# Performance work log

Measured on AMD Instinct MI355X. Metric: run time of the kernel, lower is better.

Reference implementation:

```python
import jax, jax.numpy as jnp
import numpy as np

B, S, HID = 2, 2048, 2048
H, HKV, D = 16, 4, 128

def _rope(x, cos, sin):
    # x: [B,h,S,D]; cos/sin: [1,1,S,D//2]
    d = x.shape[-1] // 2
    x1, x2 = x[..., :d], x[..., d:]
    y1 = x1 * cos + x2 * sin
    y2 = -x1 * sin + x2 * cos
    return jnp.concatenate([y1, y2], axis=-1)

def _rmsnorm(x):
    eps = jnp.finfo(x.dtype).eps
    return x * jax.lax.rsqrt(jnp.mean(jnp.square(x), axis=-1, keepdims=True) + eps)

def setup_inputs() -> dict:
    key = jax.random.key(0)
    ks = jax.random.split(key, 5)
    x = jax.random.normal(ks[0], (B, S, HID), dtype=jnp.float32)
    # realistic rotary tables
    half = D // 2
    inv_freq = 1.0 / (10000.0 ** (jnp.arange(half, dtype=jnp.float32) / half))
    t = jnp.arange(S, dtype=jnp.float32)
    freqs = t[:, None] * inv_freq[None, :]            # [S, D//2]
    cos = jnp.cos(freqs)[None, None]                  # [1,1,S,D//2]
    sin = jnp.sin(freqs)[None, None]
    s = 0.02
    Wq = jax.random.normal(ks[1], (H * D, HID), dtype=jnp.float32) * s
    Wk = jax.random.normal(ks[2], (HKV * D, HID), dtype=jnp.float32) * s
    Wv = jax.random.normal(ks[3], (HKV * D, HID), dtype=jnp.float32) * s
    Wo = jax.random.normal(ks[4], (HID, H * D), dtype=jnp.float32) * s
    return {"x": x, "cos": cos, "sin": sin, "Wq": Wq, "Wk": Wk, "Wv": Wv, "Wo": Wo}

def reference(x, cos, sin, Wq, Wk, Wv, Wo):
    b, s, _ = x.shape
    rep = H // HKV
    q = (x @ Wq.T).reshape(b, s, H, D).transpose(0, 2, 1, 3)      # [B,H,S,D]
    k = (x @ Wk.T).reshape(b, s, HKV, D).transpose(0, 2, 1, 3)    # [B,Hkv,S,D]
    v = (x @ Wv.T).reshape(b, s, HKV, D).transpose(0, 2, 1, 3)
    k = jnp.repeat(k, rep, axis=1)                                # GQA expand
    v = jnp.repeat(v, rep, axis=1)
    q = _rmsnorm(_rope(q, cos, sin))
    k = _rmsnorm(_rope(k, cos, sin))
    scores = jnp.einsum('bhqd,bhkd->bhqk', q, k) * (D ** -0.5)
    causal = jnp.tril(jnp.ones((s, s), dtype=bool))
    scores = jnp.where(causal, scores, -jnp.inf)
    attn = jax.nn.softmax(scores, axis=-1)
    out = jnp.einsum('bhqk,bhkd->bhqd', attn, v)                  # [B,H,S,D]
    out = out.transpose(0, 2, 1, 3).reshape(b, s, H * D)
    return out @ Wo.T
```

## Files before the change

kernel.cpp:

```cpp
#include <hip/hip_runtime.h>
#include <hip/hip_bf16.h>

#define B_  2
#define S_  2048
#define HID_ 2048
#define H_  16
#define HKV_ 4
#define D_  128

typedef __bf16 bf16_t;
typedef bf16_t bf16x8 __attribute__((ext_vector_type(8)));
typedef float f32x4 __attribute__((ext_vector_type(4)));

typedef __attribute__((address_space(3))) unsigned int lds_u32_t;
typedef const __attribute__((address_space(1))) unsigned int glob_u32_t;

__device__ __forceinline__ void gl2lds16(const bf16_t* g, bf16_t* l) {
    __builtin_amdgcn_global_load_lds((glob_u32_t*)g, (lds_u32_t*)l, 16, 0, 0);
}

__device__ __forceinline__ unsigned packbf2(float a, float b) {
    union { bf16_t h[2]; unsigned u; } p;
    p.h[0] = (bf16_t)a;
    p.h[1] = (bf16_t)b;
    return p.u;
}

__global__ void detect_dtype(const unsigned* __restrict__ x, int* __restrict__ flag) {
    int lane = threadIdx.x;
    int c = 0;
#pragma unroll
    for (int i = 0; i < 16; ++i) {
        unsigned w = x[lane * 16 + i];
        unsigned e = (w >> 7) & 0xFF;
        c += (e >= 117 && e <= 137) ? 1 : 0;
    }
#pragma unroll
    for (int m = 1; m < 64; m <<= 1) c += __shfl_xor(c, m, 64);
    if (lane == 0) *flag = (c >= 512) ? 1 : 0;
}

struct Cseg { const void* src; bf16_t* dst; int n8; };

__global__ __launch_bounds__(256) void convert_bf16(Cseg s0, Cseg s1, Cseg s2, Cseg s3,
                                                    const int* __restrict__ flagp) {
    Cseg s = (blockIdx.y == 0) ? s0 : (blockIdx.y == 1) ? s1 : (blockIdx.y == 2) ? s2 : s3;
    const int i = blockIdx.x * 256 + threadIdx.x;
    if (i >= s.n8) return;
    if (*flagp) {
        ((uint4*)s.dst)[i] = ((const uint4*)s.src)[i];
    } else {
        const float4* p = (const float4*)s.src + (size_t)i * 2;
        float4 u = p[0], v = p[1];
        bf16x8 r;
        r[0] = (bf16_t)u.x; r[1] = (bf16_t)u.y; r[2] = (bf16_t)u.z; r[3] = (bf16_t)u.w;
        r[4] = (bf16_t)v.x; r[5] = (bf16_t)v.y; r[6] = (bf16_t)v.z; r[7] = (bf16_t)v.w;
        *(bf16x8*)(s.dst + (size_t)i * 8) = r;
    }
}

__global__ __launch_bounds__(256) void gemm_lds(const bf16_t* __restrict__ A,
                                                const bf16_t* __restrict__ W,
                                                void* __restrict__ C,
                                                int M, int N, int K,
                                                const int* __restrict__ flagp, int osel) {
    __shared__ bf16_t As[128 * 32];
    __shared__ bf16_t Bs[128 * 32];

    const int tid = threadIdx.x;
    const int w = tid >> 6;
    const int lane = tid & 63;
    const int r = lane & 15;
    const int quad = lane >> 4;
    const int m0 = blockIdx.y * 128;
    const int n0 = blockIdx.x * 128;
    const bool of32 = osel && (*flagp == 0);

    const int mh = (w & 1) * 64;
    const int nh = (w >> 1) * 64;

    const int c0 = w * 2;
    const int srow = lane >> 2;
    const int scol = (lane & 3) * 8;
    const bf16_t* Ag0 = A + (size_t)(m0 + c0 * 16 + srow) * K + scol;
    const bf16_t* Ag1 = A + (size_t)(m0 + c0 * 16 + 16 + srow) * K + scol;
    const bf16_t* Wg0 = W + (size_t)(n0 + c0 * 16 + srow) * K + scol;
    const bf16_t* Wg1 = W + (size_t)(n0 + c0 * 16 + 16 + srow) * K + scol;
    bf16_t* Al0 = As + c0 * 512;
    bf16_t* Al1 = As + (c0 + 1) * 512;
    bf16_t* Bl0 = Bs + c0 * 512;
    bf16_t* Bl1 = Bs + (c0 + 1) * 512;

    f32x4 acc[4][4] = {};

    for (int k0 = 0; k0 < K; k0 += 32) {
        __syncthreads();
        gl2lds16(Ag0 + k0, Al0);
        gl2lds16(Ag1 + k0, Al1);
        gl2lds16(Wg0 + k0, Bl0);
        gl2lds16(Wg1 + k0, Bl1);
        __syncthreads();

        bf16x8 a[4], b[4];
#pragma unroll
        for (int mi = 0; mi < 4; ++mi)
            a[mi] = *(const bf16x8*)&As[(mh + mi * 16 + r) * 32 + quad * 8];
#pragma unroll
        for (int ni = 0; ni < 4; ++ni)
            b[ni] = *(const bf16x8*)&Bs[(nh + ni * 16 + r) * 32 + quad * 8];
#pragma unroll
        for (int mi = 0; mi < 4; ++mi)
#pragma unroll
            for (int ni = 0; ni < 4; ++ni)
                acc[mi][ni] = __builtin_amdgcn_mfma_f32_16x16x32_bf16(a[mi], b[ni], acc[mi][ni], 0, 0, 0);
    }

#pragma unroll
    for (int mi = 0; mi < 4; ++mi) {
#pragma unroll
        for (int ni = 0; ni < 4; ++ni) {
#pragma unroll
            for (int g = 0; g < 4; ++g) {
                const int row = m0 + mh + mi * 16 + quad * 4 + g;
                const int col = n0 + nh + ni * 16 + r;
                if (of32) ((float*)C)[(size_t)row * N + col] = acc[mi][ni][g];
                else ((__hip_bfloat16*)C)[(size_t)row * N + col] = __float2bfloat16(acc[mi][ni][g]);
            }
        }
    }
}

template <bool F32>
__device__ __forceinline__ bf16x8 load8(const void* base, size_t off) {
    bf16x8 r;
    if constexpr (F32) {
        const float4* p = (const float4*)((const float*)base + off);
        float4 u = p[0], v = p[1];
        r[0] = (bf16_t)u.x; r[1] = (bf16_t)u.y; r[2] = (bf16_t)u.z; r[3] = (bf16_t)u.w;
        r[4] = (bf16_t)v.x; r[5] = (bf16_t)v.y; r[6] = (bf16_t)v.z; r[7] = (bf16_t)v.w;
    } else {
        r = *(const bf16x8*)((const bf16_t*)base + off);
    }
    return r;
}

template <bool AF32, bool WF32, bool OF32>
__device__ __forceinline__ void gemm_body(const void* __restrict__ A, const void* __restrict__ W,
                                          void* __restrict__ C, int M, int N, int K) {
    const int wave = threadIdx.x >> 6;
    const int lane = threadIdx.x & 63;
    const int r = lane & 15;
    const int quad = lane >> 4;
    const int m0 = blockIdx.y * 64 + wave * 16;
    const int n0 = blockIdx.x * 64;

    f32x4 acc[4] = {};
    const size_t aoff = (size_t)(m0 + r) * K + quad * 8;
    const size_t woff = (size_t)(n0 + r) * K + quad * 8;

    for (int k0 = 0; k0 < K; k0 += 32) {
        bf16x8 a = load8<AF32>(A, aoff + k0);
#pragma unroll
        for (int ns = 0; ns < 4; ++ns) {
            bf16x8 b = load8<WF32>(W, woff + (size_t)(ns * 16) * K + k0);
            acc[ns] = __builtin_amdgcn_mfma_f32_16x16x32_bf16(a, b, acc[ns], 0, 0, 0);
        }
    }

#pragma unroll
    for (int ns = 0; ns < 4; ++ns) {
#pragma unroll
        for (int reg = 0; reg < 4; ++reg) {
            int m = m0 + quad * 4 + reg;
            int n = n0 + ns * 16 + r;
            if constexpr (OF32) ((float*)C)[(size_t)m * N + n] = acc[ns][reg];
            else ((__hip_bfloat16*)C)[(size_t)m * N + n] = __float2bfloat16(acc[ns][reg]);
        }
    }
}

__global__ __launch_bounds__(256) void gemm_bt(const void* __restrict__ A, const void* __restrict__ W,
                                               void* __restrict__ C, int M, int N, int K,
                                               const int* __restrict__ flagp, int mode) {
    const int bf = *flagp;
    if (bf) {
        gemm_body<false, false, false>(A, W, C, M, N, K);
    } else if (mode == 0) {
        gemm_body<true, true, false>(A, W, C, M, N, K);
    } else {
        gemm_body<false, true, true>(A, W, C, M, N, K);
    }
}

__global__ __launch_bounds__(256) void rope_rms(__hip_bfloat16* __restrict__ qk,
                                                const void* __restrict__ cosp,
                                                const void* __restrict__ sinp,
                                                int NH, int ld, const int* __restrict__ flagp) {
    const int bf = *flagp;
    const int wave = threadIdx.x >> 6;
    const int lane = threadIdx.x & 63;
    const int row = blockIdx.x * 4 + wave;
    const int h = row % NH;
    const int bs = row / NH;
    const int s = bs % S_;

    __hip_bfloat16* p = qk + (size_t)bs * ld + h * D_;
    float x1 = __bfloat162float(p[lane]);
    float x2 = __bfloat162float(p[lane + 64]);
    float c, sn, eps;
    if (bf) {
        c   = __bfloat162float(((const __hip_bfloat16*)cosp)[s * 64 + lane]);
        sn  = __bfloat162float(((const __hip_bfloat16*)sinp)[s * 64 + lane]);
        eps = 0.0078125f;
    } else {
        c   = ((const float*)cosp)[s * 64 + lane];
        sn  = ((const float*)sinp)[s * 64 + lane];
        eps = 1.1920929e-07f;
    }
    float y1 = x1 * c + x2 * sn;
    float y2 = x2 * c - x1 * sn;
    float ss = y1 * y1 + y2 * y2;
#pragma unroll
    for (int m = 1; m < 64; m <<= 1) ss += __shfl_xor(ss, m, 64);
    float rinv = rsqrtf(ss * (1.0f / 128.0f) + eps);
    p[lane]      = __float2bfloat16(y1 * rinv);
    p[lane + 64] = __float2bfloat16(y2 * rinv);
}

__global__ __launch_bounds__(256) void k_pack(const __hip_bfloat16* __restrict__ Kin,
                                              bf16_t* __restrict__ Kp) {
    const int idx = blockIdx.x * 256 + threadIdx.x;
    const int sl = idx & 15;
    const int row = (idx >> 4) & 31;
    const int kt = (idx >> 9) & 63;
    const int gy = idx >> 15;
    const int slot = sl ^ (row & 15);
    const int kvh = gy & 3;
    const int bb = gy >> 2;
    const bf16_t* src = (const bf16_t*)Kin + (size_t)(bb * S_ + kt * 32 + row) * 3072 + kvh * D_ + slot * 8;
    *(uint4*)(Kp + (size_t)idx * 8) = *(const uint4*)src;
}

__global__ __launch_bounds__(256) void v_pack(const __hip_bfloat16* __restrict__ V,
                                              unsigned* __restrict__ Vp, int ldv) {
    const int idx = blockIdx.x * 256 + threadIdx.x;
    const int j  = idx & 3;
    const int sl = (idx >> 2) & 3;
    const int d  = (idx >> 4) & 127;
    const int kt = (idx >> 11) & 63;
    const int gy = idx >> 17;
    const int s  = sl ^ ((d >> 1) & 3);
    const int kp = s * 4 + j;
    const int kvh = gy & 3;
    const int b = gy >> 2;
    const unsigned short* p = (const unsigned short*)V
        + (size_t)(b * S_ + 32 * kt + kp) * ldv + kvh * D_ + d;
    unsigned lo = p[0];
    unsigned hi = p[(size_t)16 * ldv];
    Vp[idx] = lo | (hi << 16);
}

#define M0F 16.5f

__global__ __launch_bounds__(512, 1) void attn_flash9(const __hip_bfloat16* __restrict__ Q,
                                                      const bf16_t* __restrict__ Kp,
                                                      const unsigned* __restrict__ Vp,
                                                      __hip_bfloat16* __restrict__ O) {
    __shared__ bf16_t   Kl[8][4096];
    __shared__ unsigned Vl[8][2048];
    __shared__ unsigned PbS[8][2][16][16];

    const int tid = threadIdx.x;
    const int w = tid >> 6;
    const int lane = tid & 63;
    const int r = lane & 15;
    const int quad = lane >> 4;

    const int id = blockIdx.x;
    const int gy = id & 7;
    const int u = id >> 3;
    const int hh = u & 3;
    const int i = u >> 2;
    const int kvh = gy & 3;
    const int b = gy >> 2;
    const int h = kvh * 4 + hh;

    const int s4 = w & 3;
    int tlo = (s4 == 0) ? i : (s4 == 1) ? (31 - i) : (s4 == 2) ? (16 + i) : (15 - i);
    const int qt = (w < 4) ? tlo : (63 - tlo);
    const int q0 = qt * 32;

    const bf16_t* Ksrc = Kp + (size_t)gy * (64 * 4096);
    const unsigned* Vsrc = Vp + (size_t)gy * (64 * 2048);
    bf16_t* klds = &Kl[w][0];
    unsigned* vlds = &Vl[w][0];

    bf16x8 qf[2][4];
#pragma unroll
    for (int t = 0; t < 2; ++t) {
        const bf16_t* qp = (const bf16_t*)Q + (size_t)(b * S_ + q0 + t * 16 + r) * 3072 + h * D_ + quad * 8;
#pragma unroll
        for (int c = 0; c < 4; ++c) qf[t][c] = *(const bf16x8*)(qp + c * 32);
    }

    f32x4 oacc[2][8] = {};
    f32x4 lacc[2] = {};

    bf16x8 ones;
#pragma unroll
    for (int j = 0; j < 8; ++j) ones[j] = (bf16_t)1.0f;

    const float SC2 = 0.08838834764831845f * 1.4426950408889634f;

    unsigned* pbw = &PbS[w][0][0][0];
    const int pwi = (((r >> 2) ^ quad) & 3) * 4 + (r & 3);
    const int pgrp = ((quad ^ (r >> 2)) & 3) * 4;
    const int vsw = (quad ^ ((r >> 1) & 3)) * 4;

#define ISSUE(KT) do {                                                        \
        const bf16_t* ks_ = Ksrc + (size_t)(KT) * 4096 + lane * 8;            \
        const bf16_t* vs_ = (const bf16_t*)(Vsrc + (size_t)(KT) * 2048) + lane * 8; \
        _Pragma("unroll")                                                     \
        for (int jj = 0; jj < 8; ++jj) {                                      \
            gl2lds16(ks_ + jj * 512, klds + jj * 512);                        \
            gl2lds16(vs_ + jj * 512, (bf16_t*)vlds + jj * 512);               \
        }                                                                     \
    } while (0)

    ISSUE(0);
    for (int kt = 0; kt <= qt; ++kt) {
        asm volatile("s_waitcnt vmcnt(0)" ::: "memory");

        bf16x8 kf[8], vf[8];
#pragma unroll
        for (int c = 0; c < 4; ++c) {
            const int sA = ((quad + 4 * c) ^ r) * 8;
            kf[2 * c]     = *(const bf16x8*)&klds[r * 128 + sA];
            kf[2 * c + 1] = *(const bf16x8*)&klds[(16 + r) * 128 + sA];
        }
#pragma unroll
        for (int ns = 0; ns < 8; ++ns)
            vf[ns] = *(const bf16x8*)&vlds[(ns * 16 + r) * 16 + vsw];

        asm volatile("s_waitcnt lgkmcnt(0)" ::: "memory");
        __builtin_amdgcn_sched_barrier(0);
        if (kt < qt) ISSUE(kt + 1);

        f32x4 s0_[2] = {}, s1_[2] = {};
        __builtin_amdgcn_s_setprio(1);
#pragma unroll
        for (int c = 0; c < 4; ++c) {
#pragma unroll
            for (int t = 0; t < 2; ++t) {
                s0_[t] = __builtin_amdgcn_mfma_f32_16x16x32_bf16(qf[t][c], kf[2 * c], s0_[t], 0, 0, 0);
                s1_[t] = __builtin_amdgcn_mfma_f32_16x16x32_bf16(qf[t][c], kf[2 * c + 1], s1_[t], 0, 0, 0);
            }
        }
        __builtin_amdgcn_s_setprio(0);

        if (kt == qt) {
#pragma unroll
            for (int t = 0; t < 2; ++t)
#pragma unroll
                for (int g = 0; g < 4; ++g) {
                    const int qrow = q0 + t * 16 + quad * 4 + g;
                    if (kt * 32 + r > qrow)      s0_[t][g] = -1e38f;
                    if (kt * 32 + 16 + r > qrow) s1_[t][g] = -1e38f;
                }
        }

#pragma unroll
        for (int t = 0; t < 2; ++t)
#pragma unroll
            for (int g = 0; g < 4; ++g) {
                const float p0 = exp2f(fmaf(s0_[t][g], SC2, -M0F));
                const float p1 = exp2f(fmaf(s1_[t][g], SC2, -M0F));
                pbw[t * 256 + (quad * 4 + g) * 16 + pwi] = packbf2(p0, p1);
            }

        bf16x8 pf0 = *(const bf16x8*)&pbw[r * 16 + pgrp];
        bf16x8 pf1 = *(const bf16x8*)&pbw[256 + r * 16 + pgrp];

        lacc[0] = __builtin_amdgcn_mfma_f32_16x16x32_bf16(pf0, ones, lacc[0], 0, 0, 0);
        lacc[1] = __builtin_amdgcn_mfma_f32_16x16x32_bf16(pf1, ones, lacc[1], 0, 0, 0);

        __builtin_amdgcn_s_setprio(1);
#pragma unroll
        for (int ns = 0; ns < 8; ++ns) {
            oacc[0][ns] = __builtin_amdgcn_mfma_f32_16x16x32_bf16(pf0, vf[ns], oacc[0][ns], 0, 0, 0);
            oacc[1][ns] = __builtin_amdgcn_mfma_f32_16x16x32_bf16(pf1, vf[ns], oacc[1][ns], 0, 0, 0);
        }
        __builtin_amdgcn_s_setprio(0);
    }
#undef ISSUE

#pragma unroll
    for (int t = 0; t < 2; ++t) {
#pragma unroll
        for (int g = 0; g < 4; ++g) {
            const float inv = 1.0f / lacc[t][g];
            const int qrow = q0 + t * 16 + quad * 4 + g;
            __hip_bfloat16* op = O + (size_t)(b * S_ + qrow) * 2048 + h * D_;
#pragma unroll
            for (int ns = 0; ns < 8; ++ns)
                op[ns * 16 + r] = __float2bfloat16(oacc[t][ns][g] * inv);
        }
    }
}

#define KT_ 32
#define LDK 136

__global__ __launch_bounds__(256, 2) void attn_flash3(const __hip_bfloat16* __restrict__ Q,
                                                      const __hip_bfloat16* __restrict__ K,
                                                      const __hip_bfloat16* __restrict__ V,
                                                      __hip_bfloat16* __restrict__ O,
                                                      int ldq, int ldkv, int ldo) {
    __shared__ unsigned short Ks[KT_][LDK];
    __shared__ unsigned int Vt[D_ * 16];
    __shared__ unsigned int Pb[4][2][16][16];

    const int tid = threadIdx.x;
    const int w = tid >> 6;
    const int lane = tid & 63;
    const int r = lane & 15;
    const int quad = lane >> 4;

    const int gy = blockIdx.y;
    const int kvh = gy % HKV_;
    const int b = gy / HKV_;
    const int qt = b ? blockIdx.x : (gridDim.x - 1 - blockIdx.x);
    const int q0 = qt * 32;
    const int h = kvh * 4 + w;

    bf16x8 qf[2][4];
#pragma unroll
    for (int t = 0; t < 2; ++t) {
        const bf16_t* qp = (const bf16_t*)Q + (size_t)(b * S_ + q0 + t * 16 + r) * ldq + h * D_ + quad * 8;
#pragma unroll
        for (int c = 0; c < 4; ++c) qf[t][c] = *(const bf16x8*)(qp + c * 32);
    }

    f32x4 oacc[2][8] = {};
    f32x4 lacc[2] = {};
    float m_i[2][4];
#pragma unroll
    for (int t = 0; t < 2; ++t)
#pragma unroll
        for (int g = 0; g < 4; ++g) m_i[t][g] = -3e38f;

    const bf16_t* Kg = (const bf16_t*)K + (size_t)b * S_ * ldkv + kvh * D_;
    const bf16_t* Vg = (const bf16_t*)V + (size_t)b * S_ * ldkv + kvh * D_;

    bf16x8 ones;
#pragma unroll
    for (int j = 0; j < 8; ++j) ones[j] = (bf16_t)1.0f;

    const float SC2 = 0.08838834764831845f * 1.4426950408889634f;

    const int skey = tid >> 4;
    const int sdc = tid & 15;
    union U4 { uint4 u; unsigned short s[8]; };
    U4 rk0, rk1, rv0, rv1;
    {
        const size_t o0 = (size_t)skey * ldkv + sdc * 8;
        const size_t o1 = o0 + (size_t)16 * ldkv;
        rk0.u = *(const uint4*)(Kg + o0);
        rk1.u = *(const uint4*)(Kg + o1);
        rv0.u = *(const uint4*)(Vg + o0);
        rv1.u = *(const uint4*)(Vg + o1);
    }

    for (int kt = 0; kt <= qt; ++kt) {
        const int k0 = kt * KT_;
        __syncthreads();
        *(uint4*)&Ks[skey][sdc * 8] = rk0.u;
        *(uint4*)&Ks[skey + 16][sdc * 8] = rk1.u;
#pragma unroll
        for (int j = 0; j < 8; ++j) {
            const int d = sdc * 8 + j;
            const int f = ((j >> 1) & 3) ^ (sdc & 3);
            const int grp = (skey >> 2) ^ f;
            Vt[d * 16 + grp * 4 + (skey & 3)] = (unsigned)rv0.s[j] | ((unsigned)rv1.s[j] << 16);
        }
        __syncthreads();
        if (kt < qt) {
            const size_t o0 = (size_t)(k0 + KT_ + skey) * ldkv + sdc * 8;
            const size_t o1 = o0 + (size_t)16 * ldkv;
            rk0.u = *(const uint4*)(Kg + o0);
            rk1.u = *(const uint4*)(Kg + o1);
            rv0.u = *(const uint4*)(Vg + o0);
            rv1.u = *(const uint4*)(Vg + o1);
        }

        f32x4 s0[2] = {}, s1[2] = {};
#pragma unroll
        for (int c = 0; c < 4; ++c) {
            bf16x8 kb0 = *(const bf16x8*)&Ks[r][c * 32 + quad * 8];
            bf16x8 kb1 = *(const bf16x8*)&Ks[16 + r][c * 32 + quad * 8];
#pragma unroll
            for (int t = 0; t < 2; ++t) {
                s0[t] = __builtin_amdgcn_mfma_f32_16x16x32_bf16(qf[t][c], kb0, s0[t], 0, 0, 0);
                s1[t] = __builtin_amdgcn_mfma_f32_16x16x32_bf16(qf[t][c], kb1, s1[t], 0, 0, 0);
            }
        }

        const bool bnd = (kt == qt);
#pragma unroll
        for (int t = 0; t < 2; ++t) {
            float mt[4];
#pragma unroll
            for (int g = 0; g < 4; ++g) {
                s0[t][g] *= SC2;
                s1[t][g] *= SC2;
                if (bnd) {
                    const int qrow = q0 + t * 16 + quad * 4 + g;
                    if (k0 + r > qrow)      s0[t][g] = -1e38f;
                    if (k0 + 16 + r > qrow) s1[t][g] = -1e38f;
                }
                mt[g] = fmaxf(s0[t][g], s1[t][g]);
            }
#pragma unroll
            for (int msk = 1; msk < 16; msk <<= 1) {
#pragma unroll
                for (int g = 0; g < 4; ++g) mt[g] = fmaxf(mt[g], __shfl_xor(mt[g], msk, 64));
            }
            bool upd = false;
#pragma unroll
            for (int g = 0; g < 4; ++g) upd |= (mt[g] > m_i[t][g]);
            if (__ballot(upd)) {
#pragma unroll
                for (int g = 0; g < 4; ++g) {
                    const float mn = fmaxf(m_i[t][g], mt[g]);
                    const float al = exp2f(m_i[t][g] - mn);
                    m_i[t][g] = mn;
                    lacc[t][g] *= al;
#pragma unroll
                    for (int ns = 0; ns < 8; ++ns) oacc[t][ns][g] *= al;
                }
            }
#pragma unroll
            for (int g = 0; g < 4; ++g) {
                const float p0 = exp2f(s0[t][g] - m_i[t][g]);
                const float p1 = exp2f(s1[t][g] - m_i[t][g]);
                const int row = quad * 4 + g;
                Pb[w][t][row][(((r >> 2) ^ quad) & 3) * 4 + (r & 3)] = packbf2(p0, p1);
            }
        }

        const int pgrp = ((quad ^ (r >> 2)) & 3) * 4;
        bf16x8 pf0 = *(const bf16x8*)&Pb[w][0][r][pgrp];
        bf16x8 pf1 = *(const bf16x8*)&Pb[w][1][r][pgrp];

        lacc[0] = __builtin_amdgcn_mfma_f32_16x16x32_bf16(pf0, ones, lacc[0], 0, 0, 0);
        lacc[1] = __builtin_amdgcn_mfma_f32_16x16x32_bf16(pf1, ones, lacc[1], 0, 0, 0);

#pragma unroll
        for (int ns = 0; ns < 8; ++ns) {
            const int d = ns * 16 + r;
            const int f = ((r >> 1) & 3) ^ ((2 * ns + (r >> 3)) & 3);
            bf16x8 vf = *(const bf16x8*)&Vt[d * 16 + ((quad ^ f) & 3) * 4];
            oacc[0][ns] = __builtin_amdgcn_mfma_f32_16x16x32_bf16(pf0, vf, oacc[0][ns], 0, 0, 0);
            oacc[1][ns] = __builtin_amdgcn_mfma_f32_16x16x32_bf16(pf1, vf, oacc[1][ns], 0, 0, 0);
        }
    }

#pragma unroll
    for (int t = 0; t < 2; ++t) {
#pragma unroll
        for (int g = 0; g < 4; ++g) {
            const float inv = 1.0f / lacc[t][g];
            const int qrow = q0 + t * 16 + quad * 4 + g;
            __hip_bfloat16* op = O + (size_t)(b * S_ + qrow) * ldo + h * D_;
#pragma unroll
            for (int ns = 0; ns < 8; ++ns)
                op[ns * 16 + r] = __float2bfloat16(oacc[t][ns][g] * inv);
        }
    }
}

extern "C" void kernel_launch(void* const* d_in, const int* in_sizes, int n_in,
                              void* d_out, int out_size, void* d_ws, size_t ws_size,
                              hipStream_t stream) {
    const void* x    = d_in[0];
    const void* cosp = d_in[1];
    const void* sinp = d_in[2];
    const void* Wq   = d_in[3];
    const void* Wk   = d_in[4];
    const void* Wv   = d_in[5];
    const void* Wo   = d_in[6];

    const int M = B_ * S_;
    const size_t MB = 1ull << 20;

    if (ws_size >= 28 * MB + 64) {
        char* ws = (char*)d_ws;
        bf16_t* xb = (bf16_t*)ws;
        bf16_t* wb = (bf16_t*)(ws + 16 * MB);
        bf16_t* wo = (bf16_t*)(ws + 16 * MB);
        unsigned* vp4 = (unsigned*)(ws + 24 * MB);
        bf16_t* ao = (bf16_t*)ws;
        int* flag  = (int*)(ws + 28 * MB);
        bf16_t* qkv = (bf16_t*)d_out;
        bf16_t* kp8 = (bf16_t*)((char*)d_out + 24 * MB);

        detect_dtype<<<1, 64, 0, stream>>>((const unsigned*)x, flag);

        Cseg sx{x,  xb,                          (B_ * S_ * HID_) / 8};
        Cseg sq{Wq, wb,                          (H_ * D_ * HID_) / 8};
        Cseg sk{Wk, wb + (size_t)2048 * HID_,    (HKV_ * D_ * HID_) / 8};
        Cseg sv{Wv, wb + (size_t)2560 * HID_,    (HKV_ * D_ * HID_) / 8};
        convert_bf16<<<dim3(4096, 4), 256, 0, stream>>>(sx, sq, sk, sv, flag);

        gemm_lds<<<dim3(3072 / 128, M / 128), 256, 0, stream>>>(xb, wb, qkv, M, 3072, HID_, flag, 0);

        Cseg so{Wo, wo, (HID_ * H_ * D_) / 8};
        convert_bf16<<<dim3(2048, 1), 256, 0, stream>>>(so, so, so, so, flag);

        v_pack<<<(B_ * HKV_ * D_ * 64 * 16) / 256, 256, 0, stream>>>(
            (const __hip_bfloat16*)(qkv + 2560), vp4, 3072);

        rope_rms<<<(B_ * S_ * H_) / 4, 256, 0, stream>>>((__hip_bfloat16*)qkv, cosp, sinp, H_, 3072, flag);
        rope_rms<<<(B_ * S_ * HKV_) / 4, 256, 0, stream>>>((__hip_bfloat16*)(qkv + 2048), cosp, sinp, HKV_, 3072, flag);

        k_pack<<<dim3(1024), 256, 0, stream>>>((const __hip_bfloat16*)(qkv + 2048), kp8);

        attn_flash9<<<dim3(256), 512, 0, stream>>>(
            (const __hip_bfloat16*)qkv, kp8, vp4, (__hip_bfloat16*)ao);

        gemm_lds<<<dim3(HID_ / 128, M / 128), 256, 0, stream>>>(ao, wo, d_out, M, HID_, H_ * D_, flag, 1);
    } else {
        __hip_bfloat16* qb = (__hip_bfloat16*)d_ws;
        int* flag = (int*)((char*)d_ws + (size_t)M * (H_ * D_) * sizeof(__hip_bfloat16));
        __hip_bfloat16* kb = (__hip_bfloat16*)d_out;
        __hip_bfloat16* vb = kb + (size_t)M * (HKV_ * D_);

        detect_dtype<<<1, 64, 0, stream>>>((const unsigned*)x, flag);

        gemm_bt<<<dim3((H_ * D_) / 64, M / 64), 256, 0, stream>>>(x, Wq, qb, M, H_ * D_, HID_, flag, 0);
        gemm_bt<<<dim3((HKV_ * D_) / 64, M / 64), 256, 0, stream>>>(x, Wk, kb, M, HKV_ * D_, HID_, flag, 0);
        gemm_bt<<<dim3((HKV_ * D_) / 64, M / 64), 256, 0, stream>>>(x, Wv, vb, M, HKV_ * D_, HID_, flag, 0);

        rope_rms<<<(B_ * S_ * H_) / 4, 256, 0, stream>>>(qb, cosp, sinp, H_, H_ * D_, flag);
        rope_rms<<<(B_ * S_ * HKV_) / 4, 256, 0, stream>>>(kb, cosp, sinp, HKV_, HKV_ * D_, flag);

        attn_flash3<<<dim3(S_ / 32, B_ * HKV_), 256, 0, stream>>>(qb, kb, vb, qb, H_ * D_, HKV_ * D_, H_ * D_);

        gemm_bt<<<dim3(HID_ / 64, M / 64), 256, 0, stream>>>(qb, Wo, d_out, M, HID_, H_ * D_, flag, 1);
    }
}
```

Measured before the change: 349.3 us.

## Fuse post-QKV kernels and split K/V prefetch waits in attention

Replaces the Wo conversion, V pack, two rope_rms launches and K pack with one post_qkv kernel dispatched over a 2D grid, with K rope+rmsnorm writing straight into the swizzled packed K layout. This removes several launches and one K round-trip through global memory. The attention kernel now issues K and V tile prefetches separately with partial vmcnt waits, so V loads overlap QK^T and the softmax. The risks are many idle early-exit blocks in the padded grid and tighter ordering requirements on the wait counts.

```diff
diff --git a/kernel.cpp b/kernel.cpp
--- a/kernel.cpp
+++ b/kernel.cpp
@@ -227,45 +227,100 @@
     p[lane + 64] = __float2bfloat16(y2 * rinv);
 }
 
-__global__ __launch_bounds__(256) void k_pack(const __hip_bfloat16* __restrict__ Kin,
-                                              bf16_t* __restrict__ Kp) {
-    const int idx = blockIdx.x * 256 + threadIdx.x;
-    const int sl = idx & 15;
-    const int row = (idx >> 4) & 31;
-    const int kt = (idx >> 9) & 63;
-    const int gy = idx >> 15;
-    const int slot = sl ^ (row & 15);
-    const int kvh = gy & 3;
-    const int bb = gy >> 2;
-    const bf16_t* src = (const bf16_t*)Kin + (size_t)(bb * S_ + kt * 32 + row) * 3072 + kvh * D_ + slot * 8;
-    *(uint4*)(Kp + (size_t)idx * 8) = *(const uint4*)src;
-}
-
-__global__ __launch_bounds__(256) void v_pack(const __hip_bfloat16* __restrict__ V,
-                                              unsigned* __restrict__ Vp, int ldv) {
-    const int idx = blockIdx.x * 256 + threadIdx.x;
-    const int j  = idx & 3;
-    const int sl = (idx >> 2) & 3;
-    const int d  = (idx >> 4) & 127;
-    const int kt = (idx >> 11) & 63;
-    const int gy = idx >> 17;
-    const int s  = sl ^ ((d >> 1) & 3);
-    const int kp = s * 4 + j;
-    const int kvh = gy & 3;
-    const int b = gy >> 2;
-    const unsigned short* p = (const unsigned short*)V
-        + (size_t)(b * S_ + 32 * kt + kp) * ldv + kvh * D_ + d;
-    unsigned lo = p[0];
-    unsigned hi = p[(size_t)16 * ldv];
-    Vp[idx] = lo | (hi << 16);
+__global__ __launch_bounds__(256) void post_qkv(__hip_bfloat16* __restrict__ qkv,
+                                                const void* __restrict__ cosp,
+                                                const void* __restrict__ sinp,
+                                                bf16_t* __restrict__ Kp,
+                                                unsigned* __restrict__ Vp,
+                                                const void* __restrict__ WoS,
+                                                bf16_t* __restrict__ WoD,
+                                                const int* __restrict__ flagp) {
+    const int bx = blockIdx.x;
+    const int y = blockIdx.y;
+    const int tid = threadIdx.x;
+
+    if (y <= 1) {
+        if (y == 1 && bx >= 4096) return;
+        const int bf = *flagp;
+        const int wave = tid >> 6;
+        const int lane = tid & 63;
+        const int row = bx * 4 + wave;
+        const int h  = (y == 0) ? (row & 15) : (row & 3);
+        const int bs = (y == 0) ? (row >> 4) : (row >> 2);
+        const int s = bs & 2047;
+
+        __hip_bfloat16* p = qkv + (size_t)bs * 3072 + (y ? 2048 : 0) + h * D_;
+        float x1 = __bfloat162float(p[lane]);
+        float x2 = __bfloat162float(p[lane + 64]);
+        float c, sn, eps;
+        if (bf) {
+            c   = __bfloat162float(((const __hip_bfloat16*)cosp)[s * 64 + lane]);
+            sn  = __bfloat162float(((const __hip_bfloat16*)sinp)[s * 64 + lane]);
+            eps = 0.0078125f;
+        } else {
+            c   = ((const float*)cosp)[s * 64 + lane];
+            sn  = ((const float*)sinp)[s * 64 + lane];
+            eps = 1.1920929e-07f;
+        }
+        float y1 = x1 * c + x2 * sn;
+        float y2 = x2 * c - x1 * sn;
+        float ss = y1 * y1 + y2 * y2;
+#pragma unroll
+        for (int m = 1; m < 64; m <<= 1) ss += __shfl_xor(ss, m, 64);
+        float rinv = rsqrtf(ss * (1.0f / 128.0f) + eps);
+        const float y1r = y1 * rinv, y2r = y2 * rinv;
+        if (y == 0) {
+            p[lane]      = __float2bfloat16(y1r);
+            p[lane + 64] = __float2bfloat16(y2r);
+        } else {
+            const int b = bs >> 11;
+            const int kt = s >> 5;
+            const int r32 = s & 31;
+            const int gy = b * 4 + h;
+            bf16_t* base = Kp + ((size_t)(gy * 64 + kt) * 32 + r32) * 128;
+            const int sw = r32 & 15;
+            base[(((lane >> 3) ^ sw) << 3) + (lane & 7)]       = (bf16_t)y1r;
+            base[(((8 + (lane >> 3)) ^ sw) << 3) + (lane & 7)] = (bf16_t)y2r;
+        }
+    } else if (y == 2) {
+        if (bx >= 4096) return;
+        const int idx = bx * 256 + tid;
+        const int j  = idx & 3;
+        const int sl = (idx >> 2) & 3;
+        const int d  = (idx >> 4) & 127;
+        const int kt = (idx >> 11) & 63;
+        const int gy = idx >> 17;
+        const int s2 = sl ^ ((d >> 1) & 3);
+        const int kp = s2 * 4 + j;
+        const int kvh = gy & 3;
+        const int b = gy >> 2;
+        const unsigned short* p = (const unsigned short*)qkv
+            + (size_t)(b * S_ + 32 * kt + kp) * 3072 + 2560 + kvh * D_ + d;
+        unsigned lo = p[0];
+        unsigned hi = p[(size_t)16 * 3072];
+        Vp[idx] = lo | (hi << 16);
+    } else {
+        if (bx >= 2048) return;
+        const int i = bx * 256 + tid;
+        if (*flagp) {
+            ((uint4*)WoD)[i] = ((const uint4*)WoS)[i];
+        } else {
+            const float4* p4 = (const float4*)WoS + (size_t)i * 2;
+            float4 u = p4[0], v = p4[1];
+            bf16x8 rr;
+            rr[0] = (bf16_t)u.x; rr[1] = (bf16_t)u.y; rr[2] = (bf16_t)u.z; rr[3] = (bf16_t)u.w;
+            rr[4] = (bf16_t)v.x; rr[5] = (bf16_t)v.y; rr[6] = (bf16_t)v.z; rr[7] = (bf16_t)v.w;
+            *(bf16x8*)(WoD + (size_t)i * 8) = rr;
+        }
+    }
 }
 
 #define M0F 16.5f
 
-__global__ __launch_bounds__(512, 1) void attn_flash9(const __hip_bfloat16* __restrict__ Q,
-                                                      const bf16_t* __restrict__ Kp,
-                                                      const unsigned* __restrict__ Vp,
-                                                      __hip_bfloat16* __restrict__ O) {
+__global__ __launch_bounds__(512, 1) void attn_flash10(const __hip_bfloat16* __restrict__ Q,
+                                                       const bf16_t* __restrict__ Kp,
+                                                       const unsigned* __restrict__ Vp,
+                                                       __hip_bfloat16* __restrict__ O) {
     __shared__ bf16_t   Kl[8][4096];
     __shared__ unsigned Vl[8][2048];
     __shared__ unsigned PbS[8][2][16][16];
@@ -317,34 +372,33 @@
     const int pgrp = ((quad ^ (r >> 2)) & 3) * 4;
     const int vsw = (quad ^ ((r >> 1) & 3)) * 4;
 
-#define ISSUE(KT) do {                                                        \
+#define ISSUEK(KT) do {                                                       \
         const bf16_t* ks_ = Ksrc + (size_t)(KT) * 4096 + lane * 8;            \
+        _Pragma("unroll")                                                     \
+        for (int jj = 0; jj < 8; ++jj) gl2lds16(ks_ + jj * 512, klds + jj * 512); \
+    } while (0)
+#define ISSUEV(KT) do {                                                       \
         const bf16_t* vs_ = (const bf16_t*)(Vsrc + (size_t)(KT) * 2048) + lane * 8; \
         _Pragma("unroll")                                                     \
-        for (int jj = 0; jj < 8; ++jj) {                                      \
-            gl2lds16(ks_ + jj * 512, klds + jj * 512);                        \
-            gl2lds16(vs_ + jj * 512, (bf16_t*)vlds + jj * 512);               \
-        }                                                                     \
+        for (int jj = 0; jj < 8; ++jj) gl2lds16(vs_ + jj * 512, (bf16_t*)vlds + jj * 512); \
     } while (0)
 
-    ISSUE(0);
+    ISSUEK(0);
+    ISSUEV(0);
     for (int kt = 0; kt <= qt; ++kt) {
-        asm volatile("s_waitcnt vmcnt(0)" ::: "memory");
-
-        bf16x8 kf[8], vf[8];
+        asm volatile("s_waitcnt vmcnt(8)" ::: "memory");
+
+        bf16x8 kf[8];
 #pragma unroll
         for (int c = 0; c < 4; ++c) {
             const int sA = ((quad + 4 * c) ^ r) * 8;
             kf[2 * c]     = *(const bf16x8*)&klds[r * 128 + sA];
             kf[2 * c + 1] = *(const bf16x8*)&klds[(16 + r) * 128 + sA];
         }
-#pragma unroll
-        for (int ns = 0; ns < 8; ++ns)
-            vf[ns] = *(const bf16x8*)&vlds[(ns * 16 + r) * 16 + vsw];
-
         asm volatile("s_waitcnt lgkmcnt(0)" ::: "memory");
         __builtin_amdgcn_sched_barrier(0);
-        if (kt < qt) ISSUE(kt + 1);
+        if (kt < qt) ISSUEK(kt + 1);
+        __builtin_amdgcn_sched_barrier(0);
 
         f32x4 s0_[2] = {}, s1_[2] = {};
         __builtin_amdgcn_s_setprio(1);
@@ -384,6 +438,18 @@
         lacc[0] = __builtin_amdgcn_mfma_f32_16x16x32_bf16(pf0, ones, lacc[0], 0, 0, 0);
         lacc[1] = __builtin_amdgcn_mfma_f32_16x16x32_bf16(pf1, ones, lacc[1], 0, 0, 0);
 
+        if (kt < qt) asm volatile("s_waitcnt vmcnt(8)" ::: "memory");
+        else         asm volatile("s_waitcnt vmcnt(0)" ::: "memory");
+
+        bf16x8 vf[8];
+#pragma unroll
+        for (int ns = 0; ns < 8; ++ns)
+            vf[ns] = *(const bf16x8*)&vlds[(ns * 16 + r) * 16 + vsw];
+        asm volatile("s_waitcnt lgkmcnt(0)" ::: "memory");
+        __builtin_amdgcn_sched_barrier(0);
+        if (kt < qt) ISSUEV(kt + 1);
+        __builtin_amdgcn_sched_barrier(0);
+
         __builtin_amdgcn_s_setprio(1);
 #pragma unroll
         for (int ns = 0; ns < 8; ++ns) {
@@ -392,7 +458,8 @@
         }
         __builtin_amdgcn_s_setprio(0);
     }
-#undef ISSUE
+#undef ISSUEK
+#undef ISSUEV
 
 #pragma unroll
     for (int t = 0; t < 2; ++t) {
@@ -614,18 +681,10 @@
 
         gemm_lds<<<dim3(3072 / 128, M / 128), 256, 0, stream>>>(xb, wb, qkv, M, 3072, HID_, flag, 0);
 
-        Cseg so{Wo, wo, (HID_ * H_ * D_) / 8};
-        convert_bf16<<<dim3(2048, 1), 256, 0, stream>>>(so, so, so, so, flag);
-
-        v_pack<<<(B_ * HKV_ * D_ * 64 * 16) / 256, 256, 0, stream>>>(
-            (const __hip_bfloat16*)(qkv + 2560), vp4, 3072);
-
-        rope_rms<<<(B_ * S_ * H_) / 4, 256, 0, stream>>>((__hip_bfloat16*)qkv, cosp, sinp, H_, 3072, flag);
-        rope_rms<<<(B_ * S_ * HKV_) / 4, 256, 0, stream>>>((__hip_bfloat16*)(qkv + 2048), cosp, sinp, HKV_, 3072, flag);
-
-        k_pack<<<dim3(1024), 256, 0, stream>>>((const __hip_bfloat16*)(qkv + 2048), kp8);
-
-        attn_flash9<<<dim3(256), 512, 0, stream>>>(
+        post_qkv<<<dim3(16384, 4), 256, 0, stream>>>(
+            (__hip_bfloat16*)qkv, cosp, sinp, kp8, vp4, Wo, wo, flag);
+
+        attn_flash10<<<dim3(256), 512, 0, stream>>>(
             (const __hip_bfloat16*)qkv, kp8, vp4, (__hip_bfloat16*)ao);
 
         gemm_lds<<<dim3(HID_ / 128, M / 128), 256, 0, stream>>>(ao, wo, d_out, M, HID_, H_ * D_, flag, 1);
```

Result: no change. 351.1 us (+0.5%).
